# Kernel tuning notes

Measured on AMD Instinct MI355X. Metric: run time of the kernel, lower is better.

The kernel has to match this reference:

```python
import jax, jax.numpy as jnp
import numpy as np

B, SQ, SKV, D = 16, 2048, 2048, 128


def setup_inputs() -> dict:
    key = jax.random.key(0)
    kq, kk, kv = jax.random.split(key, 3)
    q = jax.random.normal(kq, (B, SQ, D), dtype=jnp.float32)
    k = jax.random.normal(kk, (B, SKV, D), dtype=jnp.float32)
    v = jax.random.normal(kv, (B, SKV, D), dtype=jnp.float32)
    return {"q": q, "k": k, "v": v, "dropout_p": 0}


def reference(q, k, v, dropout_p):
    # scores = q @ k^T, scaled by 1/sqrt(d)
    scale = 1.0 / np.sqrt(q.shape[-1]).astype(np.float32)
    scores = jnp.einsum('bqd,bkd->bqk', q, k) * scale  # [B, SQ, SKV]
    attn = jax.nn.softmax(scores, axis=-1)
    # dropout with p=dropout_p (0 here -> identity; deterministic baseline)
    if dropout_p > 0:
        keep = 1.0 - dropout_p
        mask = jax.random.bernoulli(jax.random.key(42), keep, attn.shape)
        attn = jnp.where(mask, attn / keep, 0.0)
    return jnp.einsum('bqk,bkd->bqd', attn, v)
```

## Files before the change

kernel.cpp:

```cpp
#include <hip/hip_runtime.h>
#include <hip/hip_bf16.h>
#include <cstdint>
#include <cmath>

#define SQL 2048
#define SKVL 2048
#define DD 128
#define NB 16
#define QBLK 64
#define KVB 64
#define NT (SKVL / KVB)

typedef __attribute__((ext_vector_type(8))) short short8;
typedef __attribute__((ext_vector_type(4))) float f32x4;

__device__ __forceinline__ ushort f2bf(float x) {
    union { float f; uint32_t u; } v; v.f = x;
    uint32_t r = v.u + 0x7FFFu + ((v.u >> 16) & 1u);
    return (ushort)(r >> 16);
}

__global__ void convert_scale_k(const float* __restrict__ in, ushort* __restrict__ out, float scale) {
    size_t i = (size_t)blockIdx.x * blockDim.x + threadIdx.x;
    const f32x4* p = (const f32x4*)in + i * 2;
    f32x4 a = p[0], b = p[1];
    short8 o;
    o[0] = (short)f2bf(a[0] * scale);
    o[1] = (short)f2bf(a[1] * scale);
    o[2] = (short)f2bf(a[2] * scale);
    o[3] = (short)f2bf(a[3] * scale);
    o[4] = (short)f2bf(b[0] * scale);
    o[5] = (short)f2bf(b[1] * scale);
    o[6] = (short)f2bf(b[2] * scale);
    o[7] = (short)f2bf(b[3] * scale);
    *((short8*)out + i) = o;
}

__global__ void convert_k_tiled(const float* __restrict__ in, ushort* __restrict__ out) {
    int gid = blockIdx.x * blockDim.x + threadIdx.x;
    int c16 = gid & 15;
    int rg  = gid >> 4;
    int r   = rg & 63;
    int tile = rg >> 6;
    const f32x4* p = (const f32x4*)(in + (size_t)rg * DD + c16 * 8);
    f32x4 a = p[0], b = p[1];
    short8 o;
    o[0] = (short)f2bf(a[0]); o[1] = (short)f2bf(a[1]);
    o[2] = (short)f2bf(a[2]); o[3] = (short)f2bf(a[3]);
    o[4] = (short)f2bf(b[0]); o[5] = (short)f2bf(b[1]);
    o[6] = (short)f2bf(b[2]); o[7] = (short)f2bf(b[3]);
    int cs = c16 ^ (r & 7);
    *(short8*)(out + ((size_t)tile << 13) + r * 128 + cs * 8) = o;
}

__global__ void convert_vt_tiled(const float* __restrict__ v, ushort* __restrict__ vt) {
    __shared__ float tile[64][129];
    int bid = blockIdx.x;
    int kt = bid & 31;
    int b  = bid >> 5;
    int tx = threadIdx.x & 63, ty = threadIdx.x >> 6;
    const float* src = v + ((size_t)b * SKVL + (size_t)kt * 64) * DD;
#pragma unroll
    for (int r = ty; r < 64; r += 4) {
        tile[r][tx * 2]     = src[(size_t)r * DD + tx * 2];
        tile[r][tx * 2 + 1] = src[(size_t)r * DD + tx * 2 + 1];
    }
    __syncthreads();
    ushort* dst = vt + ((size_t)bid << 13);
#pragma unroll
    for (int i = 0; i < 4; ++i) {
        int q = threadIdx.x + 256 * i;
        int d = q >> 3;
        int csp = q & 7;
        int cs = csp ^ (d & 7);
        int h = cs >> 2, g = cs & 3;
        short8 o;
#pragma unroll
        for (int j = 0; j < 8; ++j) {
            int kv = h * 32 + g * 4 + (j & 3) + 16 * (j >> 2);
            o[j] = (short)f2bf(tile[kv][d]);
        }
        *(short8*)(dst + d * 64 + csp * 8) = o;
    }
}

#define GLD_LDS16(gsrc, ldst) \
    __builtin_amdgcn_global_load_lds((const __attribute__((address_space(1))) uint32_t*)(gsrc), \
                                     (__attribute__((address_space(3))) uint32_t*)(ldst), 16, 0, 0)

__global__ __launch_bounds__(256, 2) void fattn(
    const ushort* __restrict__ qb, const ushort* __restrict__ kbt,
    const ushort* __restrict__ vbt, float* __restrict__ out)
{
    __shared__ short8 kls[2][1024];
    __shared__ short8 vls[2][1024];

    int bid = blockIdx.x;
    int swz = (bid & 7) * 64 + (bid >> 3);
    int b  = swz >> 5;
    int qt = swz & 31;
    int lane = threadIdx.x & 63;
    int w = threadIdx.x >> 6;
    int g = lane >> 4;
    int qi = lane & 15;
    int rx = qi & 7;
    int qrow = qt * QBLK + w * 16 + qi;

    const ushort* ktile0 = kbt + ((size_t)(b * NT) << 13);
    const ushort* vtile0 = vbt + ((size_t)(b * NT) << 13);

    const ushort* qptr = qb + ((size_t)b * SQL + qrow) * DD;
    short8 qf[4];
#pragma unroll
    for (int ks = 0; ks < 4; ++ks)
        qf[ks] = *(const short8*)(qptr + ks * 32 + g * 8);

    f32x4 acc[8];
#pragma unroll
    for (int i = 0; i < 8; ++i) acc[i] = (f32x4)0.f;
    float m = -1e30f, lsum = 0.f;

#pragma unroll
    for (int i = 0; i < 4; ++i) {
        int off = w * 4096 + i * 1024;
        GLD_LDS16((const char*)ktile0 + off + lane * 16, (char*)&kls[0][0] + off);
        GLD_LDS16((const char*)vtile0 + off + lane * 16, (char*)&vls[0][0] + off);
    }
    __syncthreads();

    for (int t = 0; t < NT; ++t) {
        int cur = t & 1, nxt = cur ^ 1;
        if (t + 1 < NT) {
            const char* ks = (const char*)ktile0 + ((size_t)(t + 1) << 14);
            const char* vs = (const char*)vtile0 + ((size_t)(t + 1) << 14);
#pragma unroll
            for (int i = 0; i < 4; ++i) {
                int off = w * 4096 + i * 1024;
                GLD_LDS16(ks + off + lane * 16, (char*)&kls[nxt][0] + off);
                GLD_LDS16(vs + off + lane * 16, (char*)&vls[nxt][0] + off);
            }
        }
        f32x4 st[4];
#pragma unroll
        for (int sub = 0; sub < 4; ++sub) {
            f32x4 s = (f32x4)0.f;
            int r = sub * 16 + qi;
#pragma unroll
            for (int ks = 0; ks < 4; ++ks) {
                short8 kf = kls[cur][r * 16 + ((ks * 4 + g) ^ rx)];
                s = __builtin_amdgcn_mfma_f32_16x16x32_bf16(kf, qf[ks], s, 0, 0, 0);
            }
            st[sub] = s;
        }
        float tmax = st[0][0];
#pragma unroll
        for (int s = 0; s < 4; ++s)
#pragma unroll
            for (int r = 0; r < 4; ++r) tmax = fmaxf(tmax, st[s][r]);
        tmax = fmaxf(tmax, __shfl_xor(tmax, 16));
        tmax = fmaxf(tmax, __shfl_xor(tmax, 32));
        float mnew = fmaxf(m, tmax);
        float alpha = exp2f(m - mnew);
        m = mnew;
        float psum = 0.f;
        short8 pb0, pb1;
#pragma unroll
        for (int s = 0; s < 4; ++s)
#pragma unroll
            for (int r = 0; r < 4; ++r) {
                float p = exp2f(st[s][r] - m);
                psum += p;
                ushort pv = f2bf(p);
                if (s < 2) pb0[s * 4 + r] = (short)pv;
                else       pb1[(s - 2) * 4 + r] = (short)pv;
            }
        lsum = lsum * alpha + psum;
#pragma unroll
        for (int i = 0; i < 8; ++i) {
            acc[i][0] *= alpha; acc[i][1] *= alpha;
            acc[i][2] *= alpha; acc[i][3] *= alpha;
        }
#pragma unroll
        for (int dt = 0; dt < 8; ++dt) {
            int d = dt * 16 + qi;
#pragma unroll
            for (int h = 0; h < 2; ++h) {
                short8 vf = vls[cur][d * 8 + ((h * 4 + g) ^ rx)];
                acc[dt] = __builtin_amdgcn_mfma_f32_16x16x32_bf16(vf, h ? pb1 : pb0, acc[dt], 0, 0, 0);
            }
        }
        __syncthreads();
    }

    lsum += __shfl_xor(lsum, 16);
    lsum += __shfl_xor(lsum, 32);
    float inv = 1.f / lsum;
    float* optr = out + ((size_t)b * SQL + qrow) * DD + g * 4;
#pragma unroll
    for (int dt = 0; dt < 8; ++dt) {
        f32x4 o;
        o[0] = acc[dt][0] * inv; o[1] = acc[dt][1] * inv;
        o[2] = acc[dt][2] * inv; o[3] = acc[dt][3] * inv;
        *(f32x4*)(optr + dt * 16) = o;
    }
}

extern "C" void kernel_launch(void* const* d_in, const int* in_sizes, int n_in,
                              void* d_out, int out_size, void* d_ws, size_t ws_size,
                              hipStream_t stream) {
    const float* q = (const float*)d_in[0];
    const float* k = (const float*)d_in[1];
    const float* v = (const float*)d_in[2];
    float* out = (float*)d_out;

    uint8_t* w = (uint8_t*)d_ws;
    size_t tsz = (size_t)NB * SQL * DD * sizeof(ushort);
    ushort* qb  = (ushort*)w;
    ushort* kbt = (ushort*)(w + tsz);
    ushort* vbt = (ushort*)(w + 2 * tsz);

    float qscale = 1.4426950408889634f / sqrtf((float)DD);
    int n8 = NB * SQL * DD / 8;
    convert_scale_k<<<n8 / 256, 256, 0, stream>>>(q, qb, qscale);
    convert_k_tiled<<<NB * SKVL * 16 / 256, 256, 0, stream>>>(k, kbt);
    convert_vt_tiled<<<NB * (SKVL / 64), 256, 0, stream>>>(v, vbt);
    fattn<<<NB * (SQL / QBLK), 256, 0, stream>>>(qb, kbt, vbt, out);
}
```

Before: 165.7 us.

## Skip lazy softmax rescale, use packed bf16 convert, and raise MFMA priority

The online softmax now rescales the accumulators only when the running max grows by more than a threshold across the wave, so the per-tile alpha multiply of 32 accumulator values is skipped in most iterations. The manual float-to-bf16 rounding is replaced with the hardware packed v_cvt_pk_bf16_f32 instruction. s_setprio is raised around the MFMA blocks so they are favoured in the wave schedule, and the max reduction is written as a tree. The threshold bounds how large the unnormalised exponentials can grow, which adds some risk of precision loss or overflow if scores drift.

```diff
diff --git a/kernel.cpp b/kernel.cpp
--- a/kernel.cpp
+++ b/kernel.cpp
@@ -141,6 +141,7 @@
             }
         }
         f32x4 st[4];
+        __builtin_amdgcn_s_setprio(1);
 #pragma unroll
         for (int sub = 0; sub < 4; ++sub) {
             f32x4 s = (f32x4)0.f;
@@ -152,43 +153,52 @@
             }
             st[sub] = s;
         }
-        float tmax = st[0][0];
-#pragma unroll
-        for (int s = 0; s < 4; ++s)
-#pragma unroll
-            for (int r = 0; r < 4; ++r) tmax = fmaxf(tmax, st[s][r]);
+        __builtin_amdgcn_s_setprio(0);
+        float m0 = fmaxf(fmaxf(st[0][0], st[0][1]), fmaxf(st[0][2], st[0][3]));
+        float m1 = fmaxf(fmaxf(st[1][0], st[1][1]), fmaxf(st[1][2], st[1][3]));
+        float m2 = fmaxf(fmaxf(st[2][0], st[2][1]), fmaxf(st[2][2], st[2][3]));
+        float m3 = fmaxf(fmaxf(st[3][0], st[3][1]), fmaxf(st[3][2], st[3][3]));
+        float tmax = fmaxf(fmaxf(m0, m1), fmaxf(m2, m3));
         tmax = fmaxf(tmax, __shfl_xor(tmax, 16));
         tmax = fmaxf(tmax, __shfl_xor(tmax, 32));
-        float mnew = fmaxf(m, tmax);
-        float alpha = exp2f(m - mnew);
-        m = mnew;
-        float psum = 0.f;
-        short8 pb0, pb1;
-#pragma unroll
-        for (int s = 0; s < 4; ++s)
-#pragma unroll
-            for (int r = 0; r < 4; ++r) {
-                float p = exp2f(st[s][r] - m);
-                psum += p;
-                ushort pv = f2bf(p);
-                if (s < 2) pb0[s * 4 + r] = (short)pv;
-                else       pb1[(s - 2) * 4 + r] = (short)pv;
+        if (!__all(tmax - m <= 11.5f)) {
+            float mnew = fmaxf(m, tmax);
+            float alpha = exp2f(m - mnew);
+            m = mnew;
+            lsum *= alpha;
+#pragma unroll
+            for (int i = 0; i < 8; ++i) {
+                acc[i][0] *= alpha; acc[i][1] *= alpha;
+                acc[i][2] *= alpha; acc[i][3] *= alpha;
             }
-        lsum = lsum * alpha + psum;
-#pragma unroll
-        for (int i = 0; i < 8; ++i) {
-            acc[i][0] *= alpha; acc[i][1] *= alpha;
-            acc[i][2] *= alpha; acc[i][3] *= alpha;
-        }
+        }
+        float pv[16];
+        float ps[4];
+#pragma unroll
+        for (int s = 0; s < 4; ++s) {
+            pv[s * 4 + 0] = exp2f(st[s][0] - m);
+            pv[s * 4 + 1] = exp2f(st[s][1] - m);
+            pv[s * 4 + 2] = exp2f(st[s][2] - m);
+            pv[s * 4 + 3] = exp2f(st[s][3] - m);
+            ps[s] = (pv[s * 4 + 0] + pv[s * 4 + 1]) + (pv[s * 4 + 2] + pv[s * 4 + 3]);
+        }
+        lsum += (ps[0] + ps[1]) + (ps[2] + ps[3]);
+        union { short8 v; uint32_t u[4]; } P0, P1;
+#pragma unroll
+        for (int i = 0; i < 4; ++i) {
+            asm("v_cvt_pk_bf16_f32 %0, %1, %2" : "=v"(P0.u[i]) : "v"(pv[2 * i]), "v"(pv[2 * i + 1]));
+            asm("v_cvt_pk_bf16_f32 %0, %1, %2" : "=v"(P1.u[i]) : "v"(pv[8 + 2 * i]), "v"(pv[8 + 2 * i + 1]));
+        }
+        __builtin_amdgcn_s_setprio(1);
 #pragma unroll
         for (int dt = 0; dt < 8; ++dt) {
             int d = dt * 16 + qi;
-#pragma unroll
-            for (int h = 0; h < 2; ++h) {
-                short8 vf = vls[cur][d * 8 + ((h * 4 + g) ^ rx)];
-                acc[dt] = __builtin_amdgcn_mfma_f32_16x16x32_bf16(vf, h ? pb1 : pb0, acc[dt], 0, 0, 0);
-            }
-        }
+            acc[dt] = __builtin_amdgcn_mfma_f32_16x16x32_bf16(
+                vls[cur][d * 8 + (g ^ rx)], P0.v, acc[dt], 0, 0, 0);
+            acc[dt] = __builtin_amdgcn_mfma_f32_16x16x32_bf16(
+                vls[cur][d * 8 + ((4 + g) ^ rx)], P1.v, acc[dt], 0, 0, 0);
+        }
+        __builtin_amdgcn_s_setprio(0);
         __syncthreads();
     }
 
```

New measurement: 160.3 us. 1.03x faster.
